# Performance work log

Measured on AMD Instinct MI355X. Metric: run time of the kernel, lower is better.

## Reference

```python
import jax, jax.numpy as jnp
import numpy as np

N, E, H = 50000, 400000, 128
BN_EPS = 1e-5


def _bn_relu(x, g, b):
    # BatchNorm1d in training mode: biased batch variance
    m = x.mean(axis=0)
    v = jnp.var(x, axis=0)
    return jax.nn.relu((x - m) * (g / jnp.sqrt(v + BN_EPS)) + b)


def _mlp(x, W1, G1, B1, W2, G2, B2):
    # Linear(no bias) -> BN -> ReLU -> Linear(no bias) -> BN -> ReLU
    h = _bn_relu(x @ W1, G1, B1)
    return _bn_relu(h @ W2, G2, B2)


def setup_inputs() -> dict:
    key = jax.random.key(0)
    ks = jax.random.split(key, 16)
    node_rep = jax.random.normal(ks[0], (N, H), jnp.float32)
    edge_rep = jax.random.normal(ks[1], (E, H), jnp.float32)
    src = jax.random.randint(ks[2], (E,), 0, N, jnp.int32)
    dst = jax.random.randint(ks[3], (E,), 0, N, jnp.int32)
    deg = np.bincount(np.asarray(src), minlength=N) + np.bincount(np.asarray(dst), minlength=N)
    degree = jnp.asarray(deg, jnp.float32)

    def lin(k, fi, fo):
        return jax.random.normal(k, (fi, fo), jnp.float32) / np.sqrt(fi)

    def bn(k, f):
        kg, kb = jax.random.split(k)
        return (1.0 + 0.01 * jax.random.normal(kg, (f,), jnp.float32),
                0.01 * jax.random.normal(kb, (f,), jnp.float32))

    inp = dict(node_rep=node_rep, edge_rep=edge_rep, degree=degree,
               src=src, dst=dst,
               eps1=jnp.zeros((1,), jnp.float32), eps2=jnp.zeros((1,), jnp.float32))
    specs = {'n': H, 'e0': 2 * H, 'e1': H, 'e2': H}
    i = 4
    for name, fin in specs.items():
        W1 = lin(ks[i], fin, 2 * H); G1, B1 = bn(ks[i + 1], 2 * H)
        W2 = lin(ks[i + 2], 2 * H, H); G2, B2 = bn(ks[i + 3], H)
        i += 3
        inp.update({f'{name}W1': W1, f'{name}G1': G1, f'{name}B1': B1,
                    f'{name}W2': W2, f'{name}G2': G2, f'{name}B2': B2})
    return inp


def reference(node_rep, edge_rep, degree, src, dst, eps1, eps2,
              nW1, nG1, nB1, nW2, nG2, nB2,
              e0W1, e0G1, e0B1, e0W2, e0G2, e0B2,
              e1W1, e1G1, e1B1, e1W2, e1G2, e1B2,
              e2W1, e2G1, e2B1, e2W2, e2G2, e2B2):
    # node -> edge gather: sum endpoint node features per edge
    node2edge = node_rep[src] + node_rep[dst]                      # [E,H]
    # edge -> edge gather: per-node sum of incident edges, summed over endpoints
    S = (jax.ops.segment_sum(edge_rep, src, num_segments=N)
         + jax.ops.segment_sum(edge_rep, dst, num_segments=N))     # [N,H]
    edge2edge = S[src] + S[dst]                                    # [E,H]

    edge_new = _mlp(jnp.concatenate([node2edge, edge2edge], axis=-1),
                    e0W1, e0G1, e0B1, e0W2, e0G2, e0B2)
    edge_new = (1.0 + eps1) * edge_rep + edge_new                  # GIN-style residual

    edge_out = _mlp(edge_new, e1W1, e1G1, e1B1, e1W2, e1G2, e1B2)

    edge2node_e = _mlp(edge_new, e2W1, e2G1, e2B1, e2W2, e2G2, e2B2)
    # edge -> node gather: sum incident edge messages at each node
    edge2node = (jax.ops.segment_sum(edge2node_e, src, num_segments=N)
                 + jax.ops.segment_sum(edge2node_e, dst, num_segments=N))

    node_in = (1.0 + eps2 - degree[:, None]) * node_rep + edge2node
    node_out = _mlp(node_in, nW1, nG1, nB1, nW2, nG2, nB2)
    return (node_out, edge_out)
```

## Files before the change

### kernel.cpp

```cpp
#include <hip/hip_runtime.h>
#include <hip/hip_bf16.h>
#include <cstdint>

#define EDGES 400000
#define NODES 50000
#define HDIM  128

typedef unsigned short u16;
typedef __bf16 bf16x8 __attribute__((ext_vector_type(8)));
typedef float  f32x4  __attribute__((ext_vector_type(4)));

__device__ __forceinline__ float bf2f(u16 u) {
    union { uint32_t i; float f; } w; w.i = ((uint32_t)u) << 16; return w.f;
}
__device__ __forceinline__ u16 f2bf(float f) {
    union { float f; uint32_t i; } w; w.f = f;
    uint32_t x = w.i;
    uint32_t r = (x + 0x7fffu + ((x >> 16) & 1u)) >> 16;
    return (u16)r;
}
__device__ __forceinline__ uint32_t pk_bf16(float lo, float hi) {
    union { float f; uint32_t i; } a, b; a.f = lo; b.f = hi;
    uint32_t rl = (a.i + 0x7fffu + ((a.i >> 16) & 1u)) >> 16;
    uint32_t rh = (b.i + 0x7fffu + ((b.i >> 16) & 1u)) & 0xffff0000u;
    return rl | rh;
}
__device__ __forceinline__ void unpk2(uint32_t h2, float& lo, float& hi) {
    union { uint32_t i; float f; } a, b;
    a.i = h2 << 16; b.i = h2 & 0xffff0000u; lo = a.f; hi = b.f;
}
__device__ __forceinline__ uint32_t bnrelu2(uint32_t h2, float scl, float sch,
                                            float shl_, float shh) {
    float lo, hi; unpk2(h2, lo, hi);
    return pk_bf16(fmaxf(fmaf(lo, scl, shl_), 0.f),
                   fmaxf(fmaf(hi, sch, shh), 0.f));
}
__device__ __forceinline__ uint4 bnrelu8(uint4 v, const float* __restrict__ sc,
                                         const float* __restrict__ sh) {
    float4 s0 = *(const float4*)sc, s1 = *(const float4*)(sc + 4);
    float4 t0 = *(const float4*)sh, t1 = *(const float4*)(sh + 4);
    v.x = bnrelu2(v.x, s0.x, s0.y, t0.x, t0.y);
    v.y = bnrelu2(v.y, s0.z, s0.w, t0.z, t0.w);
    v.z = bnrelu2(v.z, s1.x, s1.y, t1.x, t1.y);
    v.w = bnrelu2(v.w, s1.z, s1.w, t1.z, t1.w);
    return v;
}

__global__ void wt_convert(const float* __restrict__ W, u16* __restrict__ Wt,
                           int K, int Nout) {
    int idx = blockIdx.x * 256 + threadIdx.x;
    if (idx < K * Nout) {
        int n = idx / K, k = idx - n * K;
        Wt[idx] = f2bf(W[(size_t)k * Nout + n]);
    }
}

__global__ void scatter_S(const float* __restrict__ edge_rep,
                          const int* __restrict__ src, const int* __restrict__ dst,
                          float* __restrict__ S) {
    size_t stride = (size_t)gridDim.x * blockDim.x;
    for (size_t i = (size_t)blockIdx.x * blockDim.x + threadIdx.x;
         i < (size_t)EDGES * HDIM; i += stride) {
        int e = (int)(i >> 7), h = (int)(i & 127);
        float v = edge_rep[i];
        atomicAdd(&S[(size_t)src[e] * HDIM + h], v);
        atomicAdd(&S[(size_t)dst[e] * HDIM + h], v);
    }
}

__global__ void build_x0_v(const float* __restrict__ node_rep, const float* __restrict__ S,
                           const int* __restrict__ src, const int* __restrict__ dst,
                           u16* __restrict__ X0) {
    size_t stride = (size_t)gridDim.x * blockDim.x;
    for (size_t t = (size_t)blockIdx.x * blockDim.x + threadIdx.x;
         t < (size_t)EDGES * 16; t += stride) {
        int e  = (int)(t >> 4);
        int h8 = (int)(t & 15) * 8;
        size_t so = (size_t)src[e] * HDIM + h8;
        size_t dv = (size_t)dst[e] * HDIM + h8;
        float4 a0 = *(const float4*)&node_rep[so], a1 = *(const float4*)&node_rep[so + 4];
        float4 b0 = *(const float4*)&node_rep[dv], b1 = *(const float4*)&node_rep[dv + 4];
        float4 c0 = *(const float4*)&S[so],        c1 = *(const float4*)&S[so + 4];
        float4 d0 = *(const float4*)&S[dv],        d1 = *(const float4*)&S[dv + 4];
        uint4 o1, o2;
        o1.x = pk_bf16(a0.x + b0.x, a0.y + b0.y);
        o1.y = pk_bf16(a0.z + b0.z, a0.w + b0.w);
        o1.z = pk_bf16(a1.x + b1.x, a1.y + b1.y);
        o1.w = pk_bf16(a1.z + b1.z, a1.w + b1.w);
        o2.x = pk_bf16(c0.x + d0.x, c0.y + d0.y);
        o2.y = pk_bf16(c0.z + d0.z, c0.w + d0.w);
        o2.z = pk_bf16(c1.x + d1.x, c1.y + d1.y);
        o2.w = pk_bf16(c1.z + d1.z, c1.w + d1.w);
        *(uint4*)&X0[(size_t)e * 256 + h8]       = o1;
        *(uint4*)&X0[(size_t)e * 256 + 128 + h8] = o2;
    }
}

template<int K, bool FUSE>
__global__ __launch_bounds__(256) void gemm_bn(
    const u16* __restrict__ A, const u16* __restrict__ Wt,
    u16* __restrict__ Out, float* __restrict__ stats, int M, int Nout,
    const float* __restrict__ fsc)
{
    __shared__ u16 Al[128][72];
    __shared__ u16 Bl[128][72];
    const int tid  = threadIdx.x;
    const int lane = tid & 63;
    const int w    = tid >> 6;
    const int wrow = w >> 1, wcol = w & 1;
    const int mrow0 = blockIdx.x * 128;
    const int ncol0 = blockIdx.y * 128;
    f32x4 acc[4][4] = {};

    const int srow = tid >> 3;
    const int sc8  = (tid & 7) * 8;

    for (int k0 = 0; k0 < K; k0 += 64) {
        if (k0) __syncthreads();
        #pragma unroll
        for (int p = 0; p < 4; ++p) {
            int row  = srow + p * 32;
            int grow = mrow0 + row;
            uint4 va = make_uint4(0u, 0u, 0u, 0u);
            if (grow < M) {
                va = *reinterpret_cast<const uint4*>(&A[(size_t)grow * K + k0 + sc8]);
                if (FUSE)
                    va = bnrelu8(va, &fsc[k0 + sc8], &fsc[K + k0 + sc8]);
            }
            *reinterpret_cast<uint4*>(&Al[row][sc8]) = va;
            uint4 vb = *reinterpret_cast<const uint4*>(&Wt[(size_t)(ncol0 + row) * K + k0 + sc8]);
            *reinterpret_cast<uint4*>(&Bl[row][sc8]) = vb;
        }
        __syncthreads();
        #pragma unroll
        for (int kk = 0; kk < 64; kk += 32) {
            const int lr = lane & 15;
            const int kc = kk + (lane >> 4) * 8;
            bf16x8 af[4], bfr[4];
            #pragma unroll
            for (int m = 0; m < 4; ++m)
                af[m] = *reinterpret_cast<const bf16x8*>(&Al[wrow * 64 + m * 16 + lr][kc]);
            #pragma unroll
            for (int n = 0; n < 4; ++n)
                bfr[n] = *reinterpret_cast<const bf16x8*>(&Bl[wcol * 64 + n * 16 + lr][kc]);
            #pragma unroll
            for (int m = 0; m < 4; ++m)
                #pragma unroll
                for (int n = 0; n < 4; ++n)
                    acc[m][n] = __builtin_amdgcn_mfma_f32_16x16x32_bf16(
                        af[m], bfr[n], acc[m][n], 0, 0, 0);
        }
    }

    const int lr = lane & 15, lq = lane >> 4;
    #pragma unroll
    for (int m = 0; m < 4; ++m) {
        #pragma unroll
        for (int n = 0; n < 4; ++n) {
            int col = ncol0 + wcol * 64 + n * 16 + lr;
            #pragma unroll
            for (int i = 0; i < 4; ++i) {
                int row = mrow0 + wrow * 64 + m * 16 + lq * 4 + i;
                if (row < M)
                    Out[(size_t)row * Nout + col] = f2bf(acc[m][n][i]);
            }
        }
    }
    #pragma unroll
    for (int n = 0; n < 4; ++n) {
        float s = 0.f, q = 0.f;
        #pragma unroll
        for (int m = 0; m < 4; ++m)
            #pragma unroll
            for (int i = 0; i < 4; ++i) { float v = acc[m][n][i]; s += v; q += v * v; }
        s += __shfl_xor(s, 16); s += __shfl_xor(s, 32);
        q += __shfl_xor(q, 16); q += __shfl_xor(q, 32);
        if (lq == 0) {
            int col = ncol0 + wcol * 64 + n * 16 + lr;
            atomicAdd(&stats[col], s);
            atomicAdd(&stats[Nout + col], q);
        }
    }
}

__global__ void bn_finalize(const float* __restrict__ stats, const float* __restrict__ G,
                            const float* __restrict__ Bi, float* __restrict__ scsh,
                            int Nout, float invM) {
    int j = threadIdx.x;
    if (j < Nout) {
        float mean = stats[j] * invM;
        float var  = stats[Nout + j] * invM - mean * mean;
        float sc   = G[j] / sqrtf(var + 1e-5f);
        scsh[j]        = sc;
        scsh[Nout + j] = Bi[j] - mean * sc;
    }
}

__global__ void edge_new_v(const float* __restrict__ edge_rep, const u16* __restrict__ H2,
                           const float* __restrict__ scsh, const float* __restrict__ eps1,
                           u16* __restrict__ EN) {
    float e1 = 1.0f + eps1[0];
    size_t stride = (size_t)gridDim.x * blockDim.x;
    for (size_t t = (size_t)blockIdx.x * blockDim.x + threadIdx.x;
         t < (size_t)EDGES * 16; t += stride) {
        size_t base = t * 8;
        int h8 = (int)(t & 15) * 8;
        uint4 h = *(const uint4*)&H2[base];
        h = bnrelu8(h, &scsh[h8], &scsh[128 + h8]);
        float4 r0 = *(const float4*)&edge_rep[base];
        float4 r1 = *(const float4*)&edge_rep[base + 4];
        float m0, m1, m2, m3, m4, m5, m6, m7;
        unpk2(h.x, m0, m1); unpk2(h.y, m2, m3);
        unpk2(h.z, m4, m5); unpk2(h.w, m6, m7);
        uint4 o;
        o.x = pk_bf16(fmaf(e1, r0.x, m0), fmaf(e1, r0.y, m1));
        o.y = pk_bf16(fmaf(e1, r0.z, m2), fmaf(e1, r0.w, m3));
        o.z = pk_bf16(fmaf(e1, r1.x, m4), fmaf(e1, r1.y, m5));
        o.w = pk_bf16(fmaf(e1, r1.z, m6), fmaf(e1, r1.w, m7));
        *(uint4*)&EN[base] = o;
    }
}

__global__ void affine_out_v(const u16* __restrict__ H, const float* __restrict__ scsh,
                             float* __restrict__ out, size_t t16) {
    size_t stride = (size_t)gridDim.x * blockDim.x;
    for (size_t t = (size_t)blockIdx.x * blockDim.x + threadIdx.x; t < t16; t += stride) {
        size_t base = t * 8;
        int h8 = (int)(t & 15) * 8;
        uint4 h = *(const uint4*)&H[base];
        float4 s0 = *(const float4*)&scsh[h8],       s1 = *(const float4*)&scsh[h8 + 4];
        float4 t0 = *(const float4*)&scsh[128 + h8], t1 = *(const float4*)&scsh[128 + h8 + 4];
        float v0, v1, v2, v3, v4, v5, v6, v7;
        unpk2(h.x, v0, v1); unpk2(h.y, v2, v3);
        unpk2(h.z, v4, v5); unpk2(h.w, v6, v7);
        float4 o0, o1;
        o0.x = fmaxf(fmaf(v0, s0.x, t0.x), 0.f);
        o0.y = fmaxf(fmaf(v1, s0.y, t0.y), 0.f);
        o0.z = fmaxf(fmaf(v2, s0.z, t0.z), 0.f);
        o0.w = fmaxf(fmaf(v3, s0.w, t0.w), 0.f);
        o1.x = fmaxf(fmaf(v4, s1.x, t1.x), 0.f);
        o1.y = fmaxf(fmaf(v5, s1.y, t1.y), 0.f);
        o1.z = fmaxf(fmaf(v6, s1.z, t1.z), 0.f);
        o1.w = fmaxf(fmaf(v7, s1.w, t1.w), 0.f);
        *(float4*)&out[base]     = o0;
        *(float4*)&out[base + 4] = o1;
    }
}

__global__ void scatter_e2n(const u16* __restrict__ H6, const float* __restrict__ scsh,
                            const int* __restrict__ src, const int* __restrict__ dst,
                            float* __restrict__ An) {
    size_t stride = (size_t)gridDim.x * blockDim.x;
    for (size_t i = (size_t)blockIdx.x * blockDim.x + threadIdx.x;
         i < (size_t)EDGES * HDIM; i += stride) {
        int e = (int)(i >> 7), h = (int)(i & 127);
        float m = fmaxf(bf2f(H6[i]) * scsh[h] + scsh[128 + h], 0.f);
        atomicAdd(&An[(size_t)src[e] * HDIM + h], m);
        atomicAdd(&An[(size_t)dst[e] * HDIM + h], m);
    }
}

__global__ void node_in_v(const float* __restrict__ node_rep, const float* __restrict__ An,
                          const float* __restrict__ degree, const float* __restrict__ eps2,
                          u16* __restrict__ NI) {
    float e2 = 1.0f + eps2[0];
    size_t stride = (size_t)gridDim.x * blockDim.x;
    for (size_t t = (size_t)blockIdx.x * blockDim.x + threadIdx.x;
         t < (size_t)NODES * 16; t += stride) {
        int n = (int)(t >> 4);
        size_t base = t * 8;
        float c = e2 - degree[n];
        float4 r0 = *(const float4*)&node_rep[base], r1 = *(const float4*)&node_rep[base + 4];
        float4 a0 = *(const float4*)&An[base],       a1 = *(const float4*)&An[base + 4];
        uint4 o;
        o.x = pk_bf16(fmaf(c, r0.x, a0.x), fmaf(c, r0.y, a0.y));
        o.y = pk_bf16(fmaf(c, r0.z, a0.z), fmaf(c, r0.w, a0.w));
        o.z = pk_bf16(fmaf(c, r1.x, a1.x), fmaf(c, r1.y, a1.y));
        o.w = pk_bf16(fmaf(c, r1.z, a1.z), fmaf(c, r1.w, a1.w));
        *(uint4*)&NI[base] = o;
    }
}

extern "C" void kernel_launch(void* const* d_in, const int* in_sizes, int n_in,
                              void* d_out, int out_size, void* d_ws, size_t ws_size,
                              hipStream_t stream) {
    const float* node_rep = (const float*)d_in[0];
    const float* edge_rep = (const float*)d_in[1];
    const float* degree   = (const float*)d_in[2];
    const int*   src      = (const int*)d_in[3];
    const int*   dst      = (const int*)d_in[4];
    const float* eps1     = (const float*)d_in[5];
    const float* eps2     = (const float*)d_in[6];
    const float* nW1  = (const float*)d_in[7];
    const float* nG1  = (const float*)d_in[8];
    const float* nB1  = (const float*)d_in[9];
    const float* nW2  = (const float*)d_in[10];
    const float* nG2  = (const float*)d_in[11];
    const float* nB2  = (const float*)d_in[12];
    const float* e0W1 = (const float*)d_in[13];
    const float* e0G1 = (const float*)d_in[14];
    const float* e0B1 = (const float*)d_in[15];
    const float* e0W2 = (const float*)d_in[16];
    const float* e0G2 = (const float*)d_in[17];
    const float* e0B2 = (const float*)d_in[18];
    const float* e1W1 = (const float*)d_in[19];
    const float* e1G1 = (const float*)d_in[20];
    const float* e1B1 = (const float*)d_in[21];
    const float* e1W2 = (const float*)d_in[22];
    const float* e1G2 = (const float*)d_in[23];
    const float* e1B2 = (const float*)d_in[24];
    const float* e2W1 = (const float*)d_in[25];
    const float* e2G1 = (const float*)d_in[26];
    const float* e2B1 = (const float*)d_in[27];
    const float* e2W2 = (const float*)d_in[28];
    const float* e2G2 = (const float*)d_in[29];
    const float* e2B2 = (const float*)d_in[30];

    size_t off = 0;
    auto alloc = [&](size_t bytes) -> void* {
        void* p = (char*)d_ws + off;
        off += (bytes + 255) & ~(size_t)255;
        return p;
    };
    u16*   BUF_A = (u16*)alloc((size_t)EDGES * 256 * 2);
    u16*   BUF_B = (u16*)alloc((size_t)EDGES * 256 * 2);
    u16*   BUF_C = (u16*)alloc((size_t)EDGES * 128 * 2);
    u16*   BUF_D = (u16*)alloc((size_t)EDGES * 128 * 2);
    float* S     = (float*)alloc((size_t)NODES * 128 * 4);
    float* An    = (float*)alloc((size_t)NODES * 128 * 4);
    u16*   NI    = (u16*)alloc((size_t)NODES * 128 * 2);
    u16*   H7    = (u16*)alloc((size_t)NODES * 256 * 2);
    u16*   H8    = (u16*)alloc((size_t)NODES * 128 * 2);
    u16* Wt_e0_1 = (u16*)alloc(256 * 256 * 2);
    u16* Wt_e0_2 = (u16*)alloc(128 * 256 * 2);
    u16* Wt_e1_1 = (u16*)alloc(256 * 128 * 2);
    u16* Wt_e1_2 = (u16*)alloc(128 * 256 * 2);
    u16* Wt_e2_1 = (u16*)alloc(256 * 128 * 2);
    u16* Wt_e2_2 = (u16*)alloc(128 * 256 * 2);
    u16* Wt_n_1  = (u16*)alloc(256 * 128 * 2);
    u16* Wt_n_2  = (u16*)alloc(128 * 256 * 2);
    float* stats = (float*)alloc(8 * 512 * 4);
    float* scsh  = (float*)alloc(8 * 512 * 4);
    if (off > ws_size) return;

    hipMemsetAsync(S,     0, (size_t)NODES * 128 * 4, stream);
    hipMemsetAsync(An,    0, (size_t)NODES * 128 * 4, stream);
    hipMemsetAsync(stats, 0, 8 * 512 * 4, stream);

    const int EB  = 8192;
    const int EV  = 4096;
    const int NV  = 3125;
    const float invE = 1.0f / (float)EDGES;
    const float invN = 1.0f / (float)NODES;
    const dim3 gE2(3125, 2), gE1(3125, 1), gN2(391, 2), gN1(391, 1);

    wt_convert<<<(256 * 256 + 255) / 256, 256, 0, stream>>>(e0W1, Wt_e0_1, 256, 256);
    wt_convert<<<(128 * 256 + 255) / 256, 256, 0, stream>>>(e0W2, Wt_e0_2, 256, 128);
    wt_convert<<<(256 * 128 + 255) / 256, 256, 0, stream>>>(e1W1, Wt_e1_1, 128, 256);
    wt_convert<<<(128 * 256 + 255) / 256, 256, 0, stream>>>(e1W2, Wt_e1_2, 256, 128);
    wt_convert<<<(256 * 128 + 255) / 256, 256, 0, stream>>>(e2W1, Wt_e2_1, 128, 256);
    wt_convert<<<(128 * 256 + 255) / 256, 256, 0, stream>>>(e2W2, Wt_e2_2, 256, 128);
    wt_convert<<<(256 * 128 + 255) / 256, 256, 0, stream>>>(nW1, Wt_n_1, 128, 256);
    wt_convert<<<(128 * 256 + 255) / 256, 256, 0, stream>>>(nW2, Wt_n_2, 256, 128);

    scatter_S<<<EB, 256, 0, stream>>>(edge_rep, src, dst, S);
    build_x0_v<<<EV, 256, 0, stream>>>(node_rep, S, src, dst, BUF_A);

    gemm_bn<256, false><<<gE2, 256, 0, stream>>>(BUF_A, Wt_e0_1, BUF_B, stats + 0 * 512, EDGES, 256, nullptr);
    bn_finalize<<<1, 256, 0, stream>>>(stats + 0 * 512, e0G1, e0B1, scsh + 0 * 512, 256, invE);
    gemm_bn<256, true><<<gE1, 256, 0, stream>>>(BUF_B, Wt_e0_2, BUF_C, stats + 1 * 512, EDGES, 128, scsh + 0 * 512);
    bn_finalize<<<1, 256, 0, stream>>>(stats + 1 * 512, e0G2, e0B2, scsh + 1 * 512, 128, invE);
    edge_new_v<<<EV, 256, 0, stream>>>(edge_rep, BUF_C, scsh + 1 * 512, eps1, BUF_D);

    gemm_bn<128, false><<<gE2, 256, 0, stream>>>(BUF_D, Wt_e1_1, BUF_A, stats + 2 * 512, EDGES, 256, nullptr);
    bn_finalize<<<1, 256, 0, stream>>>(stats + 2 * 512, e1G1, e1B1, scsh + 2 * 512, 256, invE);
    gemm_bn<256, true><<<gE1, 256, 0, stream>>>(BUF_A, Wt_e1_2, BUF_C, stats + 3 * 512, EDGES, 128, scsh + 2 * 512);
    bn_finalize<<<1, 256, 0, stream>>>(stats + 3 * 512, e1G2, e1B2, scsh + 3 * 512, 128, invE);
    affine_out_v<<<EV, 256, 0, stream>>>(BUF_C, scsh + 3 * 512,
                                         (float*)d_out + (size_t)NODES * HDIM,
                                         (size_t)EDGES * 16);

    gemm_bn<128, false><<<gE2, 256, 0, stream>>>(BUF_D, Wt_e2_1, BUF_B, stats + 4 * 512, EDGES, 256, nullptr);
    bn_finalize<<<1, 256, 0, stream>>>(stats + 4 * 512, e2G1, e2B1, scsh + 4 * 512, 256, invE);
    gemm_bn<256, true><<<gE1, 256, 0, stream>>>(BUF_B, Wt_e2_2, BUF_C, stats + 5 * 512, EDGES, 128, scsh + 4 * 512);
    bn_finalize<<<1, 256, 0, stream>>>(stats + 5 * 512, e2G2, e2B2, scsh + 5 * 512, 128, invE);
    scatter_e2n<<<EB, 256, 0, stream>>>(BUF_C, scsh + 5 * 512, src, dst, An);

    node_in_v<<<NV, 256, 0, stream>>>(node_rep, An, degree, eps2, NI);
    gemm_bn<128, false><<<gN2, 256, 0, stream>>>(NI, Wt_n_1, H7, stats + 6 * 512, NODES, 256, nullptr);
    bn_finalize<<<1, 256, 0, stream>>>(stats + 6 * 512, nG1, nB1, scsh + 6 * 512, 256, invN);
    gemm_bn<256, true><<<gN1, 256, 0, stream>>>(H7, Wt_n_2, H8, stats + 7 * 512, NODES, 128, scsh + 6 * 512);
    bn_finalize<<<1, 256, 0, stream>>>(stats + 7 * 512, nG2, nB2, scsh + 7 * 512, 128, invN);
    affine_out_v<<<NV, 256, 0, stream>>>(H8, scsh + 7 * 512, (float*)d_out,
                                         (size_t)NODES * 16);
}
```

Measured before the change: 2.910 ms.

## Use direct global-to-LDS loads for GEMM tiles and raise occupancy hint

Replaces the register-staged global→LDS copies of the weight tile (and of the A tile when no BN fusion is needed) with global_load_lds 16-byte direct transfers, which requires dropping the LDS row padding. It also requests 4 blocks per CU via launch bounds, and pads the node input buffer with zeros so unguarded A loads for the last partial tile stay in bounds. Removing the padding may introduce LDS bank conflicts on the MFMA fragment reads, and the occupancy hint may force register spills.

```diff
diff --git a/kernel.cpp b/kernel.cpp
--- a/kernel.cpp
+++ b/kernel.cpp
@@ -44,6 +44,12 @@
     v.z = bnrelu2(v.z, s1.x, s1.y, t1.x, t1.y);
     v.w = bnrelu2(v.w, s1.z, s1.w, t1.z, t1.w);
     return v;
+}
+
+__device__ __forceinline__ void gload16(const u16* g, u16* l) {
+    __builtin_amdgcn_global_load_lds(
+        (const __attribute__((address_space(1))) void*)(const void*)g,
+        (__attribute__((address_space(3))) void*)(void*)l, 16, 0, 0);
 }
 
 __global__ void wt_convert(const float* __restrict__ W, u16* __restrict__ Wt,
@@ -97,13 +103,13 @@
 }
 
 template<int K, bool FUSE>
-__global__ __launch_bounds__(256) void gemm_bn(
+__global__ __launch_bounds__(256, 4) void gemm_bn(
     const u16* __restrict__ A, const u16* __restrict__ Wt,
     u16* __restrict__ Out, float* __restrict__ stats, int M, int Nout,
     const float* __restrict__ fsc)
 {
-    __shared__ u16 Al[128][72];
-    __shared__ u16 Bl[128][72];
+    __shared__ u16 Al[128][64];
+    __shared__ u16 Bl[128][64];
     const int tid  = threadIdx.x;
     const int lane = tid & 63;
     const int w    = tid >> 6;
@@ -114,22 +120,34 @@
 
     const int srow = tid >> 3;
     const int sc8  = (tid & 7) * 8;
+    const int crow = lane >> 3;
+    const int cc8  = (lane & 7) * 8;
 
     for (int k0 = 0; k0 < K; k0 += 64) {
         if (k0) __syncthreads();
         #pragma unroll
-        for (int p = 0; p < 4; ++p) {
-            int row  = srow + p * 32;
-            int grow = mrow0 + row;
-            uint4 va = make_uint4(0u, 0u, 0u, 0u);
-            if (grow < M) {
-                va = *reinterpret_cast<const uint4*>(&A[(size_t)grow * K + k0 + sc8]);
-                if (FUSE)
+        for (int ch = w; ch < 16; ch += 4) {
+            int row = ch * 8 + crow;
+            gload16(&Wt[(size_t)(ncol0 + row) * K + k0 + cc8], &Bl[ch * 8][0]);
+        }
+        if (!FUSE) {
+            #pragma unroll
+            for (int ch = w; ch < 16; ch += 4) {
+                int row = ch * 8 + crow;
+                gload16(&A[(size_t)(mrow0 + row) * K + k0 + cc8], &Al[ch * 8][0]);
+            }
+        } else {
+            #pragma unroll
+            for (int p = 0; p < 4; ++p) {
+                int row  = srow + p * 32;
+                int grow = mrow0 + row;
+                uint4 va = make_uint4(0u, 0u, 0u, 0u);
+                if (grow < M) {
+                    va = *reinterpret_cast<const uint4*>(&A[(size_t)grow * K + k0 + sc8]);
                     va = bnrelu8(va, &fsc[k0 + sc8], &fsc[K + k0 + sc8]);
+                }
+                *reinterpret_cast<uint4*>(&Al[row][sc8]) = va;
             }
-            *reinterpret_cast<uint4*>(&Al[row][sc8]) = va;
-            uint4 vb = *reinterpret_cast<const uint4*>(&Wt[(size_t)(ncol0 + row) * K + k0 + sc8]);
-            *reinterpret_cast<uint4*>(&Bl[row][sc8]) = vb;
         }
         __syncthreads();
         #pragma unroll
@@ -322,13 +340,14 @@
         off += (bytes + 255) & ~(size_t)255;
         return p;
     };
+    const int NPAD = 50048;
     u16*   BUF_A = (u16*)alloc((size_t)EDGES * 256 * 2);
     u16*   BUF_B = (u16*)alloc((size_t)EDGES * 256 * 2);
     u16*   BUF_C = (u16*)alloc((size_t)EDGES * 128 * 2);
     u16*   BUF_D = (u16*)alloc((size_t)EDGES * 128 * 2);
     float* S     = (float*)alloc((size_t)NODES * 128 * 4);
     float* An    = (float*)alloc((size_t)NODES * 128 * 4);
-    u16*   NI    = (u16*)alloc((size_t)NODES * 128 * 2);
+    u16*   NI    = (u16*)alloc((size_t)NPAD * 128 * 2);
     u16*   H7    = (u16*)alloc((size_t)NODES * 256 * 2);
     u16*   H8    = (u16*)alloc((size_t)NODES * 128 * 2);
     u16* Wt_e0_1 = (u16*)alloc(256 * 256 * 2);
@@ -346,6 +365,8 @@
     hipMemsetAsync(S,     0, (size_t)NODES * 128 * 4, stream);
     hipMemsetAsync(An,    0, (size_t)NODES * 128 * 4, stream);
     hipMemsetAsync(stats, 0, 8 * 512 * 4, stream);
+    hipMemsetAsync(NI + (size_t)NODES * 128, 0,
+                   (size_t)(NPAD - NODES) * 128 * 2, stream);
 
     const int EB  = 8192;
     const int EV  = 4096;
```

Result: faster. 2.815 ms (-3.3%).
